# Performance work log

Measured on AMD Instinct MI355X. Metric: run time of the kernel, lower is better.

## Reference

```python
import jax, jax.numpy as jnp
import numpy as np


def setup_inputs() -> dict:
    key = jax.random.key(0)
    k1, k2, k3 = jax.random.split(key, 3)
    B, S, D = 4, 2048, 1024
    return {
        "enc_outputs": jax.random.normal(k1, (B, S, D), dtype=jnp.float32),
        "atten_outputs": jax.random.normal(k2, (B, S, D), dtype=jnp.float32),
        "enc_residual": jax.random.normal(k3, (B, S, D), dtype=jnp.float32),
    }


def reference(enc_outputs, atten_outputs, enc_residual):
    # score[b,q,k] = enc_outputs[b,q,:] . atten_outputs[b,k,:]  -> [B,S1,S2]
    score = jnp.einsum("bqd,bkd->bqk", enc_outputs, atten_outputs)
    alignment = jax.nn.softmax(score, axis=-1)  # over S2
    # keras dot(axes=(1,1)): contract S1 of alignment with S1 of (x0+x2) -> [B,S2,D]
    return jnp.einsum("bqk,bqd->bkd", alignment, enc_outputs + enc_residual)
```

## Files before the change

### kernel.cpp

```cpp
#include <hip/hip_runtime.h>

#define BB 4
#define SS 2048
#define DD 1024

typedef __attribute__((ext_vector_type(8))) _Float16 half8;
typedef __attribute__((ext_vector_type(4))) float f32x4;
typedef unsigned short ushort_t;

__device__ __forceinline__ ushort_t f2h(float f) {
    union { _Float16 h; ushort_t u; } c;
    c.h = (_Float16)f;
    return c.u;
}

union Pack8 { ushort_t u[8]; uint4 v; };

__global__ __launch_bounds__(256) void conv_h_qk(const float* __restrict__ enc,
                                                 const float* __restrict__ att,
                                                 ushort_t* __restrict__ Qb,
                                                 ushort_t* __restrict__ Kb) {
    const float* in = blockIdx.y ? att : enc;
    ushort_t* out   = blockIdx.y ? Kb : Qb;
    long i = ((long)blockIdx.x * 256 + threadIdx.x) * 8;
    float4 a = *(const float4*)(in + i);
    float4 b = *(const float4*)(in + i + 4);
    Pack8 p;
    p.u[0] = f2h(a.x); p.u[1] = f2h(a.y); p.u[2] = f2h(a.z); p.u[3] = f2h(a.w);
    p.u[4] = f2h(b.x); p.u[5] = f2h(b.y); p.u[6] = f2h(b.z); p.u[7] = f2h(b.w);
    *(uint4*)(out + i) = p.v;
}

__global__ __launch_bounds__(256, 2)
void gemm_bt(const ushort_t* __restrict__ A, const ushort_t* __restrict__ Bm,
             float* __restrict__ C, int M, int N, int Kd,
             long sAb, long sBb, long sCb) {
    __shared__ ushort_t Abuf[128 * 64];
    __shared__ ushort_t Bbuf[128 * 64];

    const int t = threadIdx.x;
    const int w = t >> 6, lane = t & 63;
    const int wr = w >> 1, wc = w & 1;
    const int m0 = blockIdx.x << 7;
    const int n0 = blockIdx.y << 7;
    const int bz = blockIdx.z;

    const ushort_t* Ab = A + (long)bz * sAb;
    const ushort_t* Bb = Bm + (long)bz * sBb;
    float* Cb = C + (long)bz * sCb;

    f32x4 zero = {0.f, 0.f, 0.f, 0.f};
    f32x4 acc[4][4];
    #pragma unroll
    for (int i = 0; i < 4; ++i)
        #pragma unroll
        for (int j = 0; j < 4; ++j) acc[i][j] = zero;

    const int rloc = lane >> 3;
    const int rho  = (lane & 7) << 4;

    const int nkt = Kd >> 6;
    for (int kt = 0; kt < nkt; ++kt) {
        const int k0 = kt << 6;
        __syncthreads();
        #pragma unroll
        for (int i = 0; i < 4; ++i) {
            int c = (w << 2) | i;
            int r = (c << 3) + rloc;
            int rs = rho ^ ((r & 7) << 4);
            const char* src = (const char*)(Ab + (long)(m0 + r) * Kd + k0) + rs;
            __builtin_amdgcn_global_load_lds(
                (__attribute__((address_space(1))) void*)src,
                (__attribute__((address_space(3))) void*)((char*)Abuf + (c << 10)),
                16, 0, 0);
        }
        #pragma unroll
        for (int i = 0; i < 4; ++i) {
            int c = (w << 2) | i;
            int r = (c << 3) + rloc;
            int rs = rho ^ ((r & 7) << 4);
            const char* src = (const char*)(Bb + (long)(n0 + r) * Kd + k0) + rs;
            __builtin_amdgcn_global_load_lds(
                (__attribute__((address_space(1))) void*)src,
                (__attribute__((address_space(3))) void*)((char*)Bbuf + (c << 10)),
                16, 0, 0);
        }
        __syncthreads();

        #pragma unroll
        for (int kk = 0; kk < 64; kk += 32) {
            const int colb = (kk + ((lane >> 4) << 3)) << 1;
            half8 af[4], bf[4];
            #pragma unroll
            for (int am = 0; am < 4; ++am) {
                int rA = (wr << 6) + (am << 4) + (lane & 15);
                int addr = (rA << 7) + (colb ^ ((rA & 7) << 4));
                af[am] = *(const half8*)((const char*)Abuf + addr);
            }
            #pragma unroll
            for (int bn = 0; bn < 4; ++bn) {
                int rB = (wc << 6) + (bn << 4) + (lane & 15);
                int addr = (rB << 7) + (colb ^ ((rB & 7) << 4));
                bf[bn] = *(const half8*)((const char*)Bbuf + addr);
            }
            #pragma unroll
            for (int am = 0; am < 4; ++am)
                #pragma unroll
                for (int bn = 0; bn < 4; ++bn)
                    acc[am][bn] = __builtin_amdgcn_mfma_f32_16x16x32_f16(
                        af[am], bf[bn], acc[am][bn], 0, 0, 0);
        }
    }

    #pragma unroll
    for (int am = 0; am < 4; ++am) {
        int mrow = m0 + (wr << 6) + (am << 4) + ((lane >> 4) << 2);
        #pragma unroll
        for (int bn = 0; bn < 4; ++bn) {
            int ncol = n0 + (wc << 6) + (bn << 4) + (lane & 15);
            #pragma unroll
            for (int j = 0; j < 4; ++j)
                Cb[(long)(mrow + j) * N + ncol] = acc[am][bn][j];
        }
    }
}

__device__ __forceinline__ float wred_max(float v) {
    #pragma unroll
    for (int o = 32; o > 0; o >>= 1) v = fmaxf(v, __shfl_xor(v, o, 64));
    return v;
}
__device__ __forceinline__ float wred_sum(float v) {
    #pragma unroll
    for (int o = 32; o > 0; o >>= 1) v += __shfl_xor(v, o, 64);
    return v;
}

__global__ __launch_bounds__(256) void softmax_rows(float* __restrict__ score) {
    __shared__ float red[4];
    __shared__ float bc[2];
    const long row = blockIdx.x;
    float* rp = score + row * (long)SS;
    const int t = threadIdx.x, w = t >> 6, lane = t & 63;

    float4 v0 = ((const float4*)rp)[t * 2];
    float4 v1 = ((const float4*)rp)[t * 2 + 1];
    float f[8] = {v0.x, v0.y, v0.z, v0.w, v1.x, v1.y, v1.z, v1.w};

    float m = f[0];
    #pragma unroll
    for (int j = 1; j < 8; ++j) m = fmaxf(m, f[j]);
    m = wred_max(m);
    if (lane == 0) red[w] = m;
    __syncthreads();
    if (t == 0) bc[0] = fmaxf(fmaxf(red[0], red[1]), fmaxf(red[2], red[3]));
    __syncthreads();
    m = bc[0];

    float e[8], s = 0.f;
    #pragma unroll
    for (int j = 0; j < 8; ++j) { e[j] = __expf(f[j] - m); s += e[j]; }
    s = wred_sum(s);
    if (lane == 0) red[w] = s;
    __syncthreads();
    if (t == 0) bc[1] = red[0] + red[1] + red[2] + red[3];
    __syncthreads();
    const float inv = 1.f / bc[1];

    Pack8 p;
    #pragma unroll
    for (int j = 0; j < 8; ++j) p.u[j] = f2h(e[j] * inv);
    ((uint4*)rp)[t] = p.v;
}

__global__ __launch_bounds__(256) void transposeP(const ushort_t* __restrict__ Pb,
                                                  ushort_t* __restrict__ Pt) {
    __shared__ ushort_t lds[64][72];
    const int b = blockIdx.z;
    const int n0 = blockIdx.x << 6, q0 = blockIdx.y << 6;
    const int t = threadIdx.x, rh = t >> 3, cb = (t & 7) << 3;

    #pragma unroll
    for (int it = 0; it < 2; ++it) {
        int r = (it << 5) + rh;
        const ushort_t* src = Pb + ((long)(b * SS + q0 + r)) * 4096 + n0 + cb;
        *(uint4*)&lds[r][cb] = *(const uint4*)src;
    }
    __syncthreads();
    #pragma unroll
    for (int it = 0; it < 2; ++it) {
        int rr = (it << 5) + rh;
        Pack8 p;
        #pragma unroll
        for (int j = 0; j < 8; ++j) p.u[j] = lds[cb + j][rr];
        *(uint4*)(Pt + ((long)b * SS + n0 + rr) * (long)SS + q0 + cb) = p.v;
    }
}

__global__ __launch_bounds__(256) void transposeX(const float* __restrict__ enc,
                                                  const float* __restrict__ res,
                                                  ushort_t* __restrict__ Xbt) {
    __shared__ ushort_t lds[64][72];
    const int b = blockIdx.z;
    const int q0 = blockIdx.x << 6, d0 = blockIdx.y << 6;
    const int t = threadIdx.x, rh = t >> 3, cb = (t & 7) << 3;

    #pragma unroll
    for (int it = 0; it < 2; ++it) {
        int r = (it << 5) + rh;
        long base = ((long)b * SS + q0 + r) * (long)DD + d0 + cb;
        float4 a0 = *(const float4*)(enc + base);
        float4 a1 = *(const float4*)(enc + base + 4);
        float4 b0 = *(const float4*)(res + base);
        float4 b1 = *(const float4*)(res + base + 4);
        Pack8 p;
        p.u[0] = f2h(a0.x + b0.x); p.u[1] = f2h(a0.y + b0.y);
        p.u[2] = f2h(a0.z + b0.z); p.u[3] = f2h(a0.w + b0.w);
        p.u[4] = f2h(a1.x + b1.x); p.u[5] = f2h(a1.y + b1.y);
        p.u[6] = f2h(a1.z + b1.z); p.u[7] = f2h(a1.w + b1.w);
        *(uint4*)&lds[r][cb] = p.v;
    }
    __syncthreads();
    #pragma unroll
    for (int it = 0; it < 2; ++it) {
        int rr = (it << 5) + rh;
        Pack8 p;
        #pragma unroll
        for (int j = 0; j < 8; ++j) p.u[j] = lds[cb + j][rr];
        *(uint4*)(Xbt + ((long)b * DD + d0 + rr) * (long)SS + q0 + cb) = p.v;
    }
}

extern "C" void kernel_launch(void* const* d_in, const int* in_sizes, int n_in,
                              void* d_out, int out_size, void* d_ws, size_t ws_size,
                              hipStream_t stream) {
    const float* enc = (const float*)d_in[0];
    const float* att = (const float*)d_in[1];
    const float* res = (const float*)d_in[2];
    float* out = (float*)d_out;
    char* ws = (char*)d_ws;

    float*    score = (float*)ws;
    ushort_t* Qb    = (ushort_t*)(ws + 67108864);
    ushort_t* Kb    = (ushort_t*)(ws + 67108864 + 16777216);
    ushort_t* Pt    = (ushort_t*)(ws + 67108864);
    ushort_t* Xbt   = (ushort_t*)ws;

    conv_h_qk<<<dim3(4096, 2), 256, 0, stream>>>(enc, att, Qb, Kb);

    gemm_bt<<<dim3(16, 16, BB), 256, 0, stream>>>(
        Qb, Kb, score, SS, SS, DD,
        (long)SS * DD, (long)SS * DD, (long)SS * SS);

    softmax_rows<<<BB * SS, 256, 0, stream>>>(score);

    transposeP<<<dim3(32, 32, BB), 256, 0, stream>>>((const ushort_t*)score, Pt);

    transposeX<<<dim3(32, 16, BB), 256, 0, stream>>>(enc, res, Xbt);

    gemm_bt<<<dim3(16, 8, BB), 256, 0, stream>>>(
        Pt, Xbt, out, SS, DD, SS,
        (long)SS * SS, (long)DD * SS, (long)SS * DD);
}
```

Before: 244.9 us.

## Replace GEMM with 256x128-tile, 8-wave, triple-buffered LDS pipelined kernel

Replaces the 128x128 single-buffered GEMM with a 512-thread kernel that computes 256x128 tiles. It triple-buffers LDS via global_load_lds, splitting each k-step into two phases that interleave staging with MFMA, and uses s_setprio around the MFMA block. A 1-D grid with an XCD-aware swizzle maps workgroups to tiles so neighbouring tiles share L2. The aim is to hide global load latency behind compute and raise data reuse per tile, at the cost of 144KB of LDS (one block per CU) and fragile hand-written vmcnt waits.

```diff
diff --git a/kernel.cpp b/kernel.cpp
--- a/kernel.cpp
+++ b/kernel.cpp
@@ -31,96 +31,126 @@
     *(uint4*)(out + i) = p.v;
 }
 
-__global__ __launch_bounds__(256, 2)
-void gemm_bt(const ushort_t* __restrict__ A, const ushort_t* __restrict__ Bm,
-             float* __restrict__ C, int M, int N, int Kd,
-             long sAb, long sBb, long sCb) {
-    __shared__ ushort_t Abuf[128 * 64];
-    __shared__ ushort_t Bbuf[128 * 64];
-
+#define SBUF 49152
+
+template<int NKT>
+__global__ __launch_bounds__(512, 1)
+void gemm8p(const ushort_t* __restrict__ A, const ushort_t* __restrict__ Bm,
+            float* __restrict__ C, int N, int NTN,
+            long sAb, long sBb, long sCb) {
+    extern __shared__ char lds[];
+    const int Kd = NKT * 64;
     const int t = threadIdx.x;
     const int w = t >> 6, lane = t & 63;
-    const int wr = w >> 1, wc = w & 1;
-    const int m0 = blockIdx.x << 7;
-    const int n0 = blockIdx.y << 7;
-    const int bz = blockIdx.z;
-
-    const ushort_t* Ab = A + (long)bz * sAb;
-    const ushort_t* Bb = Bm + (long)bz * sBb;
+    const int wr = w >> 2, wc = w & 3;
+
+    const int nwg = gridDim.x;
+    const int cpx = nwg >> 3;
+    const int lid = blockIdx.x;
+    const int swz = (lid & 7) * cpx + (lid >> 3);
+    const int per_b = NTN << 3;
+    const int bz  = swz / per_b;
+    const int rem = swz - bz * per_b;
+    const int m0 = (rem & 7) << 8;
+    const int n0 = (rem >> 3) << 7;
+
+    const ushort_t* Ab = A + (long)bz * sAb + (long)m0 * Kd;
+    const ushort_t* Bb = Bm + (long)bz * sBb + (long)n0 * Kd;
     float* Cb = C + (long)bz * sCb;
 
-    f32x4 zero = {0.f, 0.f, 0.f, 0.f};
-    f32x4 acc[4][4];
-    #pragma unroll
-    for (int i = 0; i < 4; ++i)
-        #pragma unroll
-        for (int j = 0; j < 4; ++j) acc[i][j] = zero;
-
-    const int rloc = lane >> 3;
-    const int rho  = (lane & 7) << 4;
-
-    const int nkt = Kd >> 6;
-    for (int kt = 0; kt < nkt; ++kt) {
-        const int k0 = kt << 6;
-        __syncthreads();
-        #pragma unroll
-        for (int i = 0; i < 4; ++i) {
-            int c = (w << 2) | i;
-            int r = (c << 3) + rloc;
-            int rs = rho ^ ((r & 7) << 4);
-            const char* src = (const char*)(Ab + (long)(m0 + r) * Kd + k0) + rs;
-            __builtin_amdgcn_global_load_lds(
-                (__attribute__((address_space(1))) void*)src,
-                (__attribute__((address_space(3))) void*)((char*)Abuf + (c << 10)),
-                16, 0, 0);
-        }
-        #pragma unroll
-        for (int i = 0; i < 4; ++i) {
-            int c = (w << 2) | i;
-            int r = (c << 3) + rloc;
-            int rs = rho ^ ((r & 7) << 4);
-            const char* src = (const char*)(Bb + (long)(n0 + r) * Kd + k0) + rs;
-            __builtin_amdgcn_global_load_lds(
-                (__attribute__((address_space(1))) void*)src,
-                (__attribute__((address_space(3))) void*)((char*)Bbuf + (c << 10)),
-                16, 0, 0);
-        }
-        __syncthreads();
-
-        #pragma unroll
-        for (int kk = 0; kk < 64; kk += 32) {
-            const int colb = (kk + ((lane >> 4) << 3)) << 1;
-            half8 af[4], bf[4];
+    f32x4 acc[8][2];
+    #pragma unroll
+    for (int i = 0; i < 8; ++i)
+        #pragma unroll
+        for (int j = 0; j < 2; ++j) acc[i][j] = f32x4{0.f, 0.f, 0.f, 0.f};
+
+    const int srow  = lane >> 3;
+    const int schnk = ((lane & 7) << 4) ^ (srow << 4);
+
+    auto STAGE_A = [&](int kt, char* bufb, int jj) {
+        int bb = jj * 8 + w;
+        int r  = bb * 8 + srow;
+        const char* src = (const char*)(Ab + (long)r * Kd + kt * 64) + schnk;
+        __builtin_amdgcn_global_load_lds(
+            (__attribute__((address_space(1))) void*)src,
+            (__attribute__((address_space(3))) void*)(bufb + (bb << 10)),
+            16, 0, 0);
+    };
+    auto STAGE_B = [&](int kt, char* bufb, int jj) {
+        int bb = jj * 8 + w;
+        int r  = bb * 8 + srow;
+        const char* src = (const char*)(Bb + (long)r * Kd + kt * 64) + schnk;
+        __builtin_amdgcn_global_load_lds(
+            (__attribute__((address_space(1))) void*)src,
+            (__attribute__((address_space(3))) void*)(bufb + 32768 + (bb << 10)),
+            16, 0, 0);
+    };
+
+    const int lar    = lane & 15;
+    const int colhib = (lane >> 4) << 4;
+
+    auto PHASE = [&](char* cb, int kk, int skt, char* sb, bool dostage, int vm) {
+        half8 af[8]; half8 bf[2];
+        const int colb = (kk << 6) | colhib;
+        #pragma unroll
+        for (int fm = 0; fm < 8; ++fm) {
+            int rA = (wr << 7) + (fm << 4) + lar;
+            af[fm] = *(const half8*)(cb + (rA << 7) + (colb ^ ((rA & 7) << 4)));
+        }
+        #pragma unroll
+        for (int fn = 0; fn < 2; ++fn) {
+            int rB = (wc << 5) + (fn << 4) + lar;
+            bf[fn] = *(const half8*)(cb + 32768 + (rB << 7) + (colb ^ ((rB & 7) << 4)));
+        }
+        if (dostage) {
+            if (kk == 0) { STAGE_A(skt, sb, 0); STAGE_A(skt, sb, 1); STAGE_B(skt, sb, 0); }
+            else         { STAGE_A(skt, sb, 2); STAGE_A(skt, sb, 3); STAGE_B(skt, sb, 1); }
+        }
+        if (vm == 6)      asm volatile("s_waitcnt vmcnt(6)" ::: "memory");
+        else if (vm == 0) asm volatile("s_waitcnt vmcnt(0)" ::: "memory");
+        __builtin_amdgcn_s_barrier();
+        __builtin_amdgcn_s_setprio(1);
+        #pragma unroll
+        for (int fm = 0; fm < 8; ++fm)
             #pragma unroll
-            for (int am = 0; am < 4; ++am) {
-                int rA = (wr << 6) + (am << 4) + (lane & 15);
-                int addr = (rA << 7) + (colb ^ ((rA & 7) << 4));
-                af[am] = *(const half8*)((const char*)Abuf + addr);
-            }
+            for (int fn = 0; fn < 2; ++fn)
+                acc[fm][fn] = __builtin_amdgcn_mfma_f32_16x16x32_f16(
+                    af[fm], bf[fn], acc[fm][fn], 0, 0, 0);
+        __builtin_amdgcn_s_setprio(0);
+        __builtin_amdgcn_s_barrier();
+    };
+
+    char* b0 = lds;
+    char* b1 = lds + SBUF;
+    char* b2 = lds + 2 * SBUF;
+    STAGE_A(0, b0, 0); STAGE_A(0, b0, 1); STAGE_A(0, b0, 2); STAGE_A(0, b0, 3);
+    STAGE_B(0, b0, 0); STAGE_B(0, b0, 1);
+    STAGE_A(1, b1, 0); STAGE_A(1, b1, 1); STAGE_A(1, b1, 2); STAGE_A(1, b1, 3);
+    STAGE_B(1, b1, 0); STAGE_B(1, b1, 1);
+    asm volatile("s_waitcnt vmcnt(6)" ::: "memory");
+    __builtin_amdgcn_s_barrier();
+
+    char *cb = b0, *nb = b1, *sb = b2;
+    for (int j = 0; j < NKT - 2; ++j) {
+        PHASE(cb, 0, j + 2, sb, true, -1);
+        PHASE(cb, 1, j + 2, sb, true, 6);
+        char* tmp = cb; cb = nb; nb = sb; sb = tmp;
+    }
+    PHASE(cb, 0, 0, sb, false, -1);
+    PHASE(cb, 1, 0, sb, false, 0);
+    { char* tmp = cb; cb = nb; nb = sb; sb = tmp; }
+    PHASE(cb, 0, 0, sb, false, -1);
+    PHASE(cb, 1, 0, sb, false, -1);
+
+    #pragma unroll
+    for (int fm = 0; fm < 8; ++fm) {
+        int mrow = m0 + (wr << 7) + (fm << 4) + ((lane >> 4) << 2);
+        #pragma unroll
+        for (int fn = 0; fn < 2; ++fn) {
+            int ncol = n0 + (wc << 5) + (fn << 4) + (lane & 15);
             #pragma unroll
-            for (int bn = 0; bn < 4; ++bn) {
-                int rB = (wc << 6) + (bn << 4) + (lane & 15);
-                int addr = (rB << 7) + (colb ^ ((rB & 7) << 4));
-                bf[bn] = *(const half8*)((const char*)Bbuf + addr);
-            }
-            #pragma unroll
-            for (int am = 0; am < 4; ++am)
-                #pragma unroll
-                for (int bn = 0; bn < 4; ++bn)
-                    acc[am][bn] = __builtin_amdgcn_mfma_f32_16x16x32_f16(
-                        af[am], bf[bn], acc[am][bn], 0, 0, 0);
-        }
-    }
-
-    #pragma unroll
-    for (int am = 0; am < 4; ++am) {
-        int mrow = m0 + (wr << 6) + (am << 4) + ((lane >> 4) << 2);
-        #pragma unroll
-        for (int bn = 0; bn < 4; ++bn) {
-            int ncol = n0 + (wc << 6) + (bn << 4) + (lane & 15);
-            #pragma unroll
-            for (int j = 0; j < 4; ++j)
-                Cb[(long)(mrow + j) * N + ncol] = acc[am][bn][j];
+            for (int q = 0; q < 4; ++q)
+                Cb[(long)(mrow + q) * N + ncol] = acc[fm][fn][q];
         }
     }
 }
@@ -246,10 +276,15 @@
     ushort_t* Pt    = (ushort_t*)(ws + 67108864);
     ushort_t* Xbt   = (ushort_t*)ws;
 
+    hipFuncSetAttribute(reinterpret_cast<const void*>(&gemm8p<16>),
+                        hipFuncAttributeMaxDynamicSharedMemorySize, 3 * SBUF);
+    hipFuncSetAttribute(reinterpret_cast<const void*>(&gemm8p<32>),
+                        hipFuncAttributeMaxDynamicSharedMemorySize, 3 * SBUF);
+
     conv_h_qk<<<dim3(4096, 2), 256, 0, stream>>>(enc, att, Qb, Kb);
 
-    gemm_bt<<<dim3(16, 16, BB), 256, 0, stream>>>(
-        Qb, Kb, score, SS, SS, DD,
+    gemm8p<16><<<512, 512, 3 * SBUF, stream>>>(
+        Qb, Kb, score, SS, 16,
         (long)SS * DD, (long)SS * DD, (long)SS * SS);
 
     softmax_rows<<<BB * SS, 256, 0, stream>>>(score);
@@ -258,7 +293,7 @@
 
     transposeX<<<dim3(32, 16, BB), 256, 0, stream>>>(enc, res, Xbt);
 
-    gemm_bt<<<dim3(16, 8, BB), 256, 0, stream>>>(
-        Pt, Xbt, out, SS, DD, SS,
+    gemm8p<32><<<256, 512, 3 * SBUF, stream>>>(
+        Pt, Xbt, out, DD, 8,
         (long)SS * SS, (long)DD * SS, (long)SS * DD);
 }
```

New measurement: 245.3 us. About the same (+0.1%).

## Compute transposed scores directly and fuse softmax with transpose via column softmax

Applied to the files above, without the earlier changes.

The first GEMM now computes K·Qᵀ so the score matrix comes out already transposed. A two-pass column softmax (online per-chunk max/sum partials, then a finalize pass that writes normalized fp16 probabilities straight into the Pt layout) replaces the row softmax and the separate transposeP kernel, removing one full read/write of the probability matrix. GEMM launches also switch to a 1D grid with an XCD-aware block swizzle (stride by 8) to improve L2 locality across chiplets. The softmax passes read the score matrix twice with strided per-thread column accesses and use few blocks (256), which may underuse bandwidth, and the partials are stashed temporarily in the output buffer.

```diff
diff --git a/kernel.cpp b/kernel.cpp
--- a/kernel.cpp
+++ b/kernel.cpp
@@ -33,7 +33,7 @@
 
 __global__ __launch_bounds__(256, 2)
 void gemm_bt(const ushort_t* __restrict__ A, const ushort_t* __restrict__ Bm,
-             float* __restrict__ C, int M, int N, int Kd,
+             float* __restrict__ C, int N, int Kd, int nmt, int nnt,
              long sAb, long sBb, long sCb) {
     __shared__ ushort_t Abuf[128 * 64];
     __shared__ ushort_t Bbuf[128 * 64];
@@ -41,9 +41,16 @@
     const int t = threadIdx.x;
     const int w = t >> 6, lane = t & 63;
     const int wr = w >> 1, wc = w & 1;
-    const int m0 = blockIdx.x << 7;
-    const int n0 = blockIdx.y << 7;
-    const int bz = blockIdx.z;
+
+    const int nwg = gridDim.x;
+    const int cpx = nwg >> 3;
+    const int lid = blockIdx.x;
+    const int swz = (lid & 7) * cpx + (lid >> 3);
+    const int per_b = nmt * nnt;
+    const int bz  = swz / per_b;
+    const int rem = swz - bz * per_b;
+    const int m0 = (rem / nnt) << 7;
+    const int n0 = (rem % nnt) << 7;
 
     const ushort_t* Ab = A + (long)bz * sAb;
     const ushort_t* Bb = Bm + (long)bz * sBb;
@@ -125,75 +132,47 @@
     }
 }
 
-__device__ __forceinline__ float wred_max(float v) {
-    #pragma unroll
-    for (int o = 32; o > 0; o >>= 1) v = fmaxf(v, __shfl_xor(v, o, 64));
-    return v;
-}
-__device__ __forceinline__ float wred_sum(float v) {
-    #pragma unroll
-    for (int o = 32; o > 0; o >>= 1) v += __shfl_xor(v, o, 64);
-    return v;
-}
-
-__global__ __launch_bounds__(256) void softmax_rows(float* __restrict__ score) {
-    __shared__ float red[4];
-    __shared__ float bc[2];
-    const long row = blockIdx.x;
-    float* rp = score + row * (long)SS;
-    const int t = threadIdx.x, w = t >> 6, lane = t & 63;
-
-    float4 v0 = ((const float4*)rp)[t * 2];
-    float4 v1 = ((const float4*)rp)[t * 2 + 1];
-    float f[8] = {v0.x, v0.y, v0.z, v0.w, v1.x, v1.y, v1.z, v1.w};
-
-    float m = f[0];
-    #pragma unroll
-    for (int j = 1; j < 8; ++j) m = fmaxf(m, f[j]);
-    m = wred_max(m);
-    if (lane == 0) red[w] = m;
-    __syncthreads();
-    if (t == 0) bc[0] = fmaxf(fmaxf(red[0], red[1]), fmaxf(red[2], red[3]));
-    __syncthreads();
-    m = bc[0];
-
-    float e[8], s = 0.f;
-    #pragma unroll
-    for (int j = 0; j < 8; ++j) { e[j] = __expf(f[j] - m); s += e[j]; }
-    s = wred_sum(s);
-    if (lane == 0) red[w] = s;
-    __syncthreads();
-    if (t == 0) bc[1] = red[0] + red[1] + red[2] + red[3];
-    __syncthreads();
-    const float inv = 1.f / bc[1];
-
-    Pack8 p;
-    #pragma unroll
-    for (int j = 0; j < 8; ++j) p.u[j] = f2h(e[j] * inv);
-    ((uint4*)rp)[t] = p.v;
-}
-
-__global__ __launch_bounds__(256) void transposeP(const ushort_t* __restrict__ Pb,
-                                                  ushort_t* __restrict__ Pt) {
-    __shared__ ushort_t lds[64][72];
-    const int b = blockIdx.z;
-    const int n0 = blockIdx.x << 6, q0 = blockIdx.y << 6;
-    const int t = threadIdx.x, rh = t >> 3, cb = (t & 7) << 3;
-
-    #pragma unroll
-    for (int it = 0; it < 2; ++it) {
-        int r = (it << 5) + rh;
-        const ushort_t* src = Pb + ((long)(b * SS + q0 + r)) * 4096 + n0 + cb;
-        *(uint4*)&lds[r][cb] = *(const uint4*)src;
-    }
-    __syncthreads();
-    #pragma unroll
-    for (int it = 0; it < 2; ++it) {
-        int rr = (it << 5) + rh;
-        Pack8 p;
-        #pragma unroll
-        for (int j = 0; j < 8; ++j) p.u[j] = lds[cb + j][rr];
-        *(uint4*)(Pt + ((long)b * SS + n0 + rr) * (long)SS + q0 + cb) = p.v;
+__global__ __launch_bounds__(256) void sm_part(const float* __restrict__ st,
+                                               float* __restrict__ pm,
+                                               float* __restrict__ pz) {
+    const int b = blockIdx.z, kc = blockIdx.y;
+    const int q = (blockIdx.x << 8) + threadIdx.x;
+    const float* base = st + ((long)b * SS + (kc << 8)) * SS + q;
+    float m = -3.4e38f, Z = 0.f;
+    #pragma unroll 8
+    for (int k = 0; k < 256; ++k) {
+        float v = base[(long)k * SS];
+        float nm = fmaxf(m, v);
+        Z = Z * __expf(m - nm) + __expf(v - nm);
+        m = nm;
+    }
+    const long idx = ((long)b * 8 + kc) * SS + q;
+    pm[idx] = m;
+    pz[idx] = Z;
+}
+
+__global__ __launch_bounds__(256) void sm_final(const float* __restrict__ st,
+                                                const float* __restrict__ pm,
+                                                const float* __restrict__ pz,
+                                                ushort_t* __restrict__ Pt) {
+    const int b = blockIdx.z, kc = blockIdx.y;
+    const int q = (blockIdx.x << 8) + threadIdx.x;
+    float m = -3.4e38f, Z = 0.f;
+    #pragma unroll
+    for (int c = 0; c < 8; ++c) {
+        const long idx = ((long)b * 8 + c) * SS + q;
+        float m2 = pm[idx], z2 = pz[idx];
+        float nm = fmaxf(m, m2);
+        Z = Z * __expf(m - nm) + z2 * __expf(m2 - nm);
+        m = nm;
+    }
+    const float inv = 1.f / Z;
+    const float* base = st + ((long)b * SS + (kc << 8)) * SS + q;
+    ushort_t*    dst  = Pt + ((long)b * SS + (kc << 8)) * SS + q;
+    #pragma unroll 8
+    for (int k = 0; k < 256; ++k) {
+        float v = base[(long)k * SS];
+        dst[(long)k * SS] = f2h(__expf(v - m) * inv);
     }
 }
 
@@ -242,23 +221,24 @@
 
     float*    score = (float*)ws;
     ushort_t* Qb    = (ushort_t*)(ws + 67108864);
-    ushort_t* Kb    = (ushort_t*)(ws + 67108864 + 16777216);
+    ushort_t* Kb    = (ushort_t*)(ws + 83886080);
     ushort_t* Pt    = (ushort_t*)(ws + 67108864);
+    float*    pm    = (float*)d_out;
+    float*    pz    = ((float*)d_out) + 65536;
     ushort_t* Xbt   = (ushort_t*)ws;
 
     conv_h_qk<<<dim3(4096, 2), 256, 0, stream>>>(enc, att, Qb, Kb);
 
-    gemm_bt<<<dim3(16, 16, BB), 256, 0, stream>>>(
-        Qb, Kb, score, SS, SS, DD,
+    gemm_bt<<<1024, 256, 0, stream>>>(
+        Kb, Qb, score, SS, DD, 16, 16,
         (long)SS * DD, (long)SS * DD, (long)SS * SS);
 
-    softmax_rows<<<BB * SS, 256, 0, stream>>>(score);
-
-    transposeP<<<dim3(32, 32, BB), 256, 0, stream>>>((const ushort_t*)score, Pt);
+    sm_part<<<dim3(8, 8, BB), 256, 0, stream>>>(score, pm, pz);
+    sm_final<<<dim3(8, 8, BB), 256, 0, stream>>>(score, pm, pz, Pt);
 
     transposeX<<<dim3(32, 16, BB), 256, 0, stream>>>(enc, res, Xbt);
 
-    gemm_bt<<<dim3(16, 8, BB), 256, 0, stream>>>(
-        Pt, Xbt, out, SS, DD, SS,
+    gemm_bt<<<512, 256, 0, stream>>>(
+        Pt, Xbt, out, DD, SS, 16, 8,
         (long)SS * SS, (long)DD * SS, (long)SS * DD);
 }
```

After: 258.6 us. +5.6%, slower.

## Store attention scores in fp16 and fuse input conversion with X transpose

Applied to the files above, without the earlier changes.

The QK GEMM now writes scores as fp16 instead of fp32, and the softmax reads fp16. This halves score memory traffic and workspace. The separate Q/K conversion and X transpose kernels are merged into one prep kernel, so enc is read once and one launch is removed. Storing raw logits in fp16 risks precision loss or overflow for large scores.

```diff
diff --git a/kernel.cpp b/kernel.cpp
--- a/kernel.cpp
+++ b/kernel.cpp
@@ -13,27 +13,63 @@
     c.h = (_Float16)f;
     return c.u;
 }
+__device__ __forceinline__ float h2f(ushort_t u) {
+    union { ushort_t u; _Float16 h; } c;
+    c.u = u;
+    return (float)c.h;
+}
 
 union Pack8 { ushort_t u[8]; uint4 v; };
 
-__global__ __launch_bounds__(256) void conv_h_qk(const float* __restrict__ enc,
-                                                 const float* __restrict__ att,
-                                                 ushort_t* __restrict__ Qb,
-                                                 ushort_t* __restrict__ Kb) {
-    const float* in = blockIdx.y ? att : enc;
-    ushort_t* out   = blockIdx.y ? Kb : Qb;
-    long i = ((long)blockIdx.x * 256 + threadIdx.x) * 8;
-    float4 a = *(const float4*)(in + i);
-    float4 b = *(const float4*)(in + i + 4);
-    Pack8 p;
-    p.u[0] = f2h(a.x); p.u[1] = f2h(a.y); p.u[2] = f2h(a.z); p.u[3] = f2h(a.w);
-    p.u[4] = f2h(b.x); p.u[5] = f2h(b.y); p.u[6] = f2h(b.z); p.u[7] = f2h(b.w);
-    *(uint4*)(out + i) = p.v;
-}
-
+__global__ __launch_bounds__(256) void prep(const float* __restrict__ enc,
+                                            const float* __restrict__ att,
+                                            const float* __restrict__ res,
+                                            ushort_t* __restrict__ Qb,
+                                            ushort_t* __restrict__ Kb,
+                                            ushort_t* __restrict__ Xbt) {
+    __shared__ ushort_t lds[64][72];
+    const int b = blockIdx.z;
+    const int q0 = blockIdx.x << 6, d0 = blockIdx.y << 6;
+    const int t = threadIdx.x, rh = t >> 3, cb = (t & 7) << 3;
+
+    #pragma unroll
+    for (int it = 0; it < 2; ++it) {
+        int r = (it << 5) + rh;
+        long base = ((long)b * SS + q0 + r) * (long)DD + d0 + cb;
+        float4 e0 = *(const float4*)(enc + base);
+        float4 e1 = *(const float4*)(enc + base + 4);
+        float4 a0 = *(const float4*)(att + base);
+        float4 a1 = *(const float4*)(att + base + 4);
+        float4 r0 = *(const float4*)(res + base);
+        float4 r1 = *(const float4*)(res + base + 4);
+        Pack8 pq, pk, px;
+        pq.u[0] = f2h(e0.x); pq.u[1] = f2h(e0.y); pq.u[2] = f2h(e0.z); pq.u[3] = f2h(e0.w);
+        pq.u[4] = f2h(e1.x); pq.u[5] = f2h(e1.y); pq.u[6] = f2h(e1.z); pq.u[7] = f2h(e1.w);
+        pk.u[0] = f2h(a0.x); pk.u[1] = f2h(a0.y); pk.u[2] = f2h(a0.z); pk.u[3] = f2h(a0.w);
+        pk.u[4] = f2h(a1.x); pk.u[5] = f2h(a1.y); pk.u[6] = f2h(a1.z); pk.u[7] = f2h(a1.w);
+        px.u[0] = f2h(e0.x + r0.x); px.u[1] = f2h(e0.y + r0.y);
+        px.u[2] = f2h(e0.z + r0.z); px.u[3] = f2h(e0.w + r0.w);
+        px.u[4] = f2h(e1.x + r1.x); px.u[5] = f2h(e1.y + r1.y);
+        px.u[6] = f2h(e1.z + r1.z); px.u[7] = f2h(e1.w + r1.w);
+        *(uint4*)(Qb + base) = pq.v;
+        *(uint4*)(Kb + base) = pk.v;
+        *(uint4*)&lds[r][cb] = px.v;
+    }
+    __syncthreads();
+    #pragma unroll
+    for (int it = 0; it < 2; ++it) {
+        int rr = (it << 5) + rh;
+        Pack8 p;
+        #pragma unroll
+        for (int j = 0; j < 8; ++j) p.u[j] = lds[cb + j][rr];
+        *(uint4*)(Xbt + ((long)b * DD + d0 + rr) * (long)SS + q0 + cb) = p.v;
+    }
+}
+
+template<int HOUT>
 __global__ __launch_bounds__(256, 2)
 void gemm_bt(const ushort_t* __restrict__ A, const ushort_t* __restrict__ Bm,
-             float* __restrict__ C, int M, int N, int Kd,
+             void* __restrict__ Cv, int N, int Kd,
              long sAb, long sBb, long sCb) {
     __shared__ ushort_t Abuf[128 * 64];
     __shared__ ushort_t Bbuf[128 * 64];
@@ -47,7 +83,6 @@
 
     const ushort_t* Ab = A + (long)bz * sAb;
     const ushort_t* Bb = Bm + (long)bz * sBb;
-    float* Cb = C + (long)bz * sCb;
 
     f32x4 zero = {0.f, 0.f, 0.f, 0.f};
     f32x4 acc[4][4];
@@ -118,9 +153,17 @@
         #pragma unroll
         for (int bn = 0; bn < 4; ++bn) {
             int ncol = n0 + (wc << 6) + (bn << 4) + (lane & 15);
-            #pragma unroll
-            for (int j = 0; j < 4; ++j)
-                Cb[(long)(mrow + j) * N + ncol] = acc[am][bn][j];
+            if (HOUT) {
+                ushort_t* Ch = (ushort_t*)Cv + (long)bz * sCb;
+                #pragma unroll
+                for (int j = 0; j < 4; ++j)
+                    Ch[(long)(mrow + j) * N + ncol] = f2h(acc[am][bn][j]);
+            } else {
+                float* Cf = (float*)Cv + (long)bz * sCb;
+                #pragma unroll
+                for (int j = 0; j < 4; ++j)
+                    Cf[(long)(mrow + j) * N + ncol] = acc[am][bn][j];
+            }
         }
     }
 }
@@ -136,16 +179,18 @@
     return v;
 }
 
-__global__ __launch_bounds__(256) void softmax_rows(float* __restrict__ score) {
+__global__ __launch_bounds__(256) void softmax_h(ushort_t* __restrict__ score) {
     __shared__ float red[4];
     __shared__ float bc[2];
     const long row = blockIdx.x;
-    float* rp = score + row * (long)SS;
+    ushort_t* rp = score + row * (long)SS;
     const int t = threadIdx.x, w = t >> 6, lane = t & 63;
 
-    float4 v0 = ((const float4*)rp)[t * 2];
-    float4 v1 = ((const float4*)rp)[t * 2 + 1];
-    float f[8] = {v0.x, v0.y, v0.z, v0.w, v1.x, v1.y, v1.z, v1.w};
+    Pack8 in;
+    in.v = ((const uint4*)rp)[t];
+    float f[8];
+    #pragma unroll
+    for (int j = 0; j < 8; ++j) f[j] = h2f(in.u[j]);
 
     float m = f[0];
     #pragma unroll
@@ -183,7 +228,7 @@
     #pragma unroll
     for (int it = 0; it < 2; ++it) {
         int r = (it << 5) + rh;
-        const ushort_t* src = Pb + ((long)(b * SS + q0 + r)) * 4096 + n0 + cb;
+        const ushort_t* src = Pb + ((long)(b * SS + q0 + r)) * SS + n0 + cb;
         *(uint4*)&lds[r][cb] = *(const uint4*)src;
     }
     __syncthreads();
@@ -194,40 +239,6 @@
         #pragma unroll
         for (int j = 0; j < 8; ++j) p.u[j] = lds[cb + j][rr];
         *(uint4*)(Pt + ((long)b * SS + n0 + rr) * (long)SS + q0 + cb) = p.v;
-    }
-}
-
-__global__ __launch_bounds__(256) void transposeX(const float* __restrict__ enc,
-                                                  const float* __restrict__ res,
-                                                  ushort_t* __restrict__ Xbt) {
-    __shared__ ushort_t lds[64][72];
-    const int b = blockIdx.z;
-    const int q0 = blockIdx.x << 6, d0 = blockIdx.y << 6;
-    const int t = threadIdx.x, rh = t >> 3, cb = (t & 7) << 3;
-
-    #pragma unroll
-    for (int it = 0; it < 2; ++it) {
-        int r = (it << 5) + rh;
-        long base = ((long)b * SS + q0 + r) * (long)DD + d0 + cb;
-        float4 a0 = *(const float4*)(enc + base);
-        float4 a1 = *(const float4*)(enc + base + 4);
-        float4 b0 = *(const float4*)(res + base);
-        float4 b1 = *(const float4*)(res + base + 4);
-        Pack8 p;
-        p.u[0] = f2h(a0.x + b0.x); p.u[1] = f2h(a0.y + b0.y);
-        p.u[2] = f2h(a0.z + b0.z); p.u[3] = f2h(a0.w + b0.w);
-        p.u[4] = f2h(a1.x + b1.x); p.u[5] = f2h(a1.y + b1.y);
-        p.u[6] = f2h(a1.z + b1.z); p.u[7] = f2h(a1.w + b1.w);
-        *(uint4*)&lds[r][cb] = p.v;
-    }
-    __syncthreads();
-    #pragma unroll
-    for (int it = 0; it < 2; ++it) {
-        int rr = (it << 5) + rh;
-        Pack8 p;
-        #pragma unroll
-        for (int j = 0; j < 8; ++j) p.u[j] = lds[cb + j][rr];
-        *(uint4*)(Xbt + ((long)b * DD + d0 + rr) * (long)SS + q0 + cb) = p.v;
     }
 }
 
@@ -237,28 +248,25 @@
     const float* enc = (const float*)d_in[0];
     const float* att = (const float*)d_in[1];
     const float* res = (const float*)d_in[2];
-    float* out = (float*)d_out;
     char* ws = (char*)d_ws;
 
-    float*    score = (float*)ws;
-    ushort_t* Qb    = (ushort_t*)(ws + 67108864);
-    ushort_t* Kb    = (ushort_t*)(ws + 67108864 + 16777216);
-    ushort_t* Pt    = (ushort_t*)(ws + 67108864);
-    ushort_t* Xbt   = (ushort_t*)ws;
-
-    conv_h_qk<<<dim3(4096, 2), 256, 0, stream>>>(enc, att, Qb, Kb);
-
-    gemm_bt<<<dim3(16, 16, BB), 256, 0, stream>>>(
-        Qb, Kb, score, SS, SS, DD,
+    ushort_t* score = (ushort_t*)ws;
+    ushort_t* Qb    = (ushort_t*)(ws + 33554432);
+    ushort_t* Kb    = (ushort_t*)(ws + 50331648);
+    ushort_t* Pt    = (ushort_t*)(ws + 33554432);
+    ushort_t* Xbt   = (ushort_t*)(ws + 67108864);
+
+    prep<<<dim3(32, 16, BB), 256, 0, stream>>>(enc, att, res, Qb, Kb, Xbt);
+
+    gemm_bt<1><<<dim3(16, 16, BB), 256, 0, stream>>>(
+        Qb, Kb, (void*)score, SS, DD,
         (long)SS * DD, (long)SS * DD, (long)SS * SS);
 
-    softmax_rows<<<BB * SS, 256, 0, stream>>>(score);
-
-    transposeP<<<dim3(32, 32, BB), 256, 0, stream>>>((const ushort_t*)score, Pt);
-
-    transposeX<<<dim3(32, 16, BB), 256, 0, stream>>>(enc, res, Xbt);
-
-    gemm_bt<<<dim3(16, 8, BB), 256, 0, stream>>>(
-        Pt, Xbt, out, SS, DD, SS,
+    softmax_h<<<BB * SS, 256, 0, stream>>>(score);
+
+    transposeP<<<dim3(32, 32, BB), 256, 0, stream>>>(score, Pt);
+
+    gemm_bt<0><<<dim3(16, 8, BB), 256, 0, stream>>>(
+        Pt, Xbt, d_out, DD, SS,
         (long)SS * SS, (long)DD * SS, (long)SS * DD);
 }
```

Measured after the change: 236.7 us. 1.03x faster.
